# Performance work log

Hardware: AMD Instinct MI355X
Metric: run time of the kernel (lower is better)

Reference implementation:

```python
import jax, jax.numpy as jnp
import numpy as np

NUM_CLASSES = 4
SMOOTH = 1e-05
W_DICE, W_CE, W_BOUND = 1.0, 1.0, 0.01
BIG = 1e8  # effectively-infinite squared distance


def _edt_sq_pass(f, axis):
    # Exact 1D squared-distance transform along `axis` via min-plus:
    # out[i] = min_j f[j] + (i-j)^2  (brute-force O(n^2), fully vectorized)
    n = f.shape[axis]
    i = jnp.arange(n, dtype=f.dtype)
    d2 = (i[:, None] - i[None, :]) ** 2  # [n, n]
    fm = jnp.moveaxis(f, axis, -1)
    out = jnp.min(fm[..., None, :] + d2, axis=-1)
    return jnp.moveaxis(out, -1, axis)


def _edt(zero_mask):
    # Euclidean distance to the nearest True voxel of zero_mask
    # (equivalent to scipy distance_transform_edt(~zero_mask)'s convention:
    #  distance to nearest zero of the input == nearest True of zero_mask).
    f = jnp.where(zero_mask, 0.0, BIG).astype(jnp.float32)
    for ax in range(f.ndim):
        f = _edt_sq_pass(f, ax)
    return jnp.sqrt(f)


def _signed_distance(mask):
    # mask: bool [D,H,W]; signed distance map: + outside, - inside.
    d_out = _edt(mask)            # distance(1 - mask)
    d_in = _edt(~mask)            # distance(mask)
    sdf = d_out - d_in
    total = jnp.sum(mask)
    size = mask.size
    sdf = jnp.where(total == 0, jnp.ones_like(sdf), sdf)
    sdf = jnp.where(total == size, -jnp.ones_like(sdf), sdf)
    return sdf


def setup_inputs() -> dict:
    key = jax.random.key(0)
    k1, k2 = jax.random.split(key)
    preds = jax.random.normal(k1, (4, NUM_CLASSES, 64, 64, 64), dtype=jnp.float32)
    targets = jax.random.randint(k2, (4, 64, 64, 64), 0, NUM_CLASSES, dtype=jnp.int32)
    return {"preds": preds, "targets": targets}


def reference(preds, targets):
    B = preds.shape[0]
    probs = jax.nn.softmax(preds, axis=1)  # [B,C,D,H,W]

    # --- Soft Dice ---
    onehot = jax.nn.one_hot(targets, NUM_CLASSES, dtype=preds.dtype)  # [B,D,H,W,C]
    onehot = jnp.moveaxis(onehot, -1, 1)  # [B,C,D,H,W]
    inter = jnp.sum(probs * onehot, axis=(2, 3, 4))
    union = jnp.sum(probs, axis=(2, 3, 4)) + jnp.sum(onehot, axis=(2, 3, 4))
    dice = (2.0 * inter + SMOOTH) / (union + SMOOTH)
    l_dice = 1.0 - jnp.mean(dice)

    # --- Cross entropy (mean over all voxels) ---
    logp = jax.nn.log_softmax(preds, axis=1)
    picked = jnp.take_along_axis(logp, targets[:, None].astype(jnp.int32), axis=1)
    l_ce = -jnp.mean(picked)

    # --- Boundary loss (classes 1..C-1) ---
    l_bound = jnp.float32(0.0)
    for c in range(1, NUM_CLASSES):
        mask_c = targets == c  # [B,D,H,W]
        sdf_c = jax.vmap(_signed_distance)(mask_c)  # [B,D,H,W]
        l_bound = l_bound + jnp.sum(jnp.mean(sdf_c * probs[:, c], axis=(1, 2, 3)))
    l_bound = l_bound / (B * (NUM_CLASSES - 1))

    return W_DICE * l_dice + W_CE * l_ce + W_BOUND * l_bound
```

## Files before the change

### kernel.cpp

```cpp
#include <hip/hip_runtime.h>
#include <hip/hip_bf16.h>
#include <math.h>

#define NVOX 262144
#define BIGF 1e8f

__device__ __forceinline__ unsigned short f2bf(float x) {
    __hip_bfloat16 h = __float2bfloat16(x);
    return *reinterpret_cast<unsigned short*>(&h);
}
__device__ __forceinline__ float bf2f(unsigned short u) {
    __hip_bfloat16 h = *reinterpret_cast<__hip_bfloat16*>(&u);
    return __bfloat162float(h);
}
__device__ __forceinline__ unsigned short dist2_u16(unsigned long long mask, int w) {
    if (mask == 0ull) return 0xFFFFu;
    unsigned long long mr = mask >> w;
    unsigned long long ml = mask << (63 - w);
    int dr = mr ? __builtin_ctzll(mr) : 127;
    int dl = ml ? __builtin_clzll(ml) : 127;
    int dd = dr < dl ? dr : dl;
    return (unsigned short)(dd * dd);
}

__global__ __launch_bounds__(256) void kA_stats_probs(
    const float* __restrict__ preds, const int* __restrict__ targets,
    unsigned short* __restrict__ probsT, float* __restrict__ part_stats) {
    __shared__ float sred[4 * 13];
    int blk = blockIdx.x;
    int b = blk >> 8, seg = blk & 255;
    int t = threadIdx.x, lane = t & 63, wid = t >> 6;
    size_t vbase = (size_t)seg * 1024 + 4 * t;
    const float* p = preds + (size_t)(b * 4) * NVOX + vbase;
    float4 x0 = *(const float4*)(p);
    float4 x1 = *(const float4*)(p + NVOX);
    float4 x2 = *(const float4*)(p + 2 * NVOX);
    float4 x3 = *(const float4*)(p + 3 * NVOX);
    int4 tv4 = *(const int4*)(targets + (size_t)b * NVOX + vbase);

    float q[13];
    #pragma unroll
    for (int k = 0; k < 13; ++k) q[k] = 0.0f;
    unsigned short pb[3][4];

    #pragma unroll
    for (int j = 0; j < 4; ++j) {
        float a0 = (&x0.x)[j], a1 = (&x1.x)[j], a2 = (&x2.x)[j], a3 = (&x3.x)[j];
        int tv = (&tv4.x)[j];
        float m  = fmaxf(fmaxf(a0, a1), fmaxf(a2, a3));
        float e0 = expf(a0 - m), e1 = expf(a1 - m), e2 = expf(a2 - m), e3 = expf(a3 - m);
        float ssum = e0 + e1 + e2 + e3;
        float inv  = 1.0f / ssum;
        float p0 = e0 * inv, p1 = e1 * inv, p2 = e2 * inv, p3 = e3 * inv;
        float xt = (tv == 0) ? a0 : (tv == 1) ? a1 : (tv == 2) ? a2 : a3;
        q[12] += -(xt - m - logf(ssum));
        q[4] += p0; q[5] += p1; q[6] += p2; q[7] += p3;
        if (tv == 0)      { q[0] += p0; q[8]  += 1.0f; }
        else if (tv == 1) { q[1] += p1; q[9]  += 1.0f; }
        else if (tv == 2) { q[2] += p2; q[10] += 1.0f; }
        else              { q[3] += p3; q[11] += 1.0f; }
        pb[0][j] = f2bf(p1); pb[1][j] = f2bf(p2); pb[2][j] = f2bf(p3);
    }

    int v0 = (int)vbase;
    int d = v0 >> 12, h = (v0 >> 6) & 63, w0 = v0 & 63;
    size_t poff = (size_t)h * 4096 + d * 64 + w0;
    #pragma unroll
    for (int c = 0; c < 3; ++c) {
        ushort4 u = make_ushort4(pb[c][0], pb[c][1], pb[c][2], pb[c][3]);
        *(ushort4*)(probsT + (size_t)(b * 3 + c) * NVOX + poff) = u;
    }

    #pragma unroll
    for (int k = 0; k < 13; ++k) {
        float x = q[k];
        #pragma unroll
        for (int o = 32; o > 0; o >>= 1) x += __shfl_down(x, o);
        if (lane == 0) sred[wid * 13 + k] = x;
    }
    __syncthreads();
    if (t < 13) {
        float s = sred[t] + sred[13 + t] + sred[26 + t] + sred[39 + t];
        part_stats[t * 1024 + blk] = s;
    }
}

__global__ __launch_bounds__(256) void kB_edt12(
    const int* __restrict__ targets, unsigned short* __restrict__ bufA) {
    __shared__ float tO[64 * 65];
    __shared__ float tI[64 * 65];
    int blk = blockIdx.x;
    int cm = blk % 3;
    int bd = blk / 3;
    int d = bd & 63, b = bd >> 6;
    int c = cm + 1;
    int t = threadIdx.x, lane = t & 63, wid = t >> 6;
    const int* tg = targets + (size_t)b * NVOX + (size_t)d * 4096;

    #pragma unroll
    for (int i = 0; i < 16; ++i) {
        int e = t + 256 * i;
        int h = wid + 4 * i;
        int tv = tg[e];
        unsigned long long mask = __ballot(tv == c);
        unsigned short o  = dist2_u16(mask, lane);
        unsigned short ii = dist2_u16(~mask, lane);
        tO[h * 65 + lane] = (o  == 0xFFFFu) ? BIGF : (float)o;
        tI[h * 65 + lane] = (ii == 0xFFFFu) ? BIGF : (float)ii;
    }
    __syncthreads();

    float hf = (float)lane;
    for (int r = 0; r < 16; ++r) {
        int w = wid * 16 + r;
        {
            float best = tO[lane * 65 + w];
            for (int dk = 1; dk < 64; ++dk) {
                float d2 = (float)(dk * dk);
                if (__all(d2 >= best)) break;
                int hl = lane - dk; hl = hl < 0 ? 0 : hl;
                int hr = lane + dk; hr = hr > 63 ? 63 : hr;
                best = fminf(fminf(best, tO[hl * 65 + w] + d2), tO[hr * 65 + w] + d2);
            }
            tO[lane * 65 + w] = best;
        }
        {
            float best = tI[lane * 65 + w];
            for (int dk = 1; dk < 64; ++dk) {
                float d2 = (float)(dk * dk);
                if (__all(d2 >= best)) break;
                int hl = lane - dk; hl = hl < 0 ? 0 : hl;
                int hr = lane + dk; hr = hr > 63 ? 63 : hr;
                best = fminf(fminf(best, tI[hl * 65 + w] + d2), tI[hr * 65 + w] + d2);
            }
            tI[lane * 65 + w] = best;
        }
    }
    __syncthreads();

    int combo = b * 3 + cm;
    size_t oO = (size_t)combo * NVOX + (size_t)d * 64;
    size_t oI = (size_t)(combo + 12) * NVOX + (size_t)d * 64;
    #pragma unroll
    for (int i = 0; i < 16; ++i) {
        int h = wid + 4 * i;
        float vo = tO[h * 65 + lane];
        float vi = tI[h * 65 + lane];
        bufA[oO + (size_t)h * 4096 + lane] = (vo >= 1e7f) ? 0xFFFFu : (unsigned short)vo;
        bufA[oI + (size_t)h * 4096 + lane] = (vi >= 1e7f) ? 0xFFFFu : (unsigned short)vi;
    }
}

__global__ __launch_bounds__(512) void k2_edt3_sdf(
    const unsigned short* __restrict__ bufA, const unsigned short* __restrict__ probsT,
    float* __restrict__ part_bound) {
    __shared__ float pl[2][64 * 65];
    __shared__ float sredb[8];
    int blk = blockIdx.x;
    int combo = blk >> 6, h = blk & 63;
    int t = threadIdx.x, lane = t & 63, wid = t >> 6;

    for (int v = 0; v < 2; ++v) {
        const unsigned short* src = bufA + (size_t)(combo + 12 * v) * NVOX + (size_t)h * 4096;
        #pragma unroll
        for (int i = 0; i < 8; ++i) {
            int e = t + 512 * i;
            unsigned short u = src[e];
            pl[v][e + (e >> 6)] = (u == 0xFFFFu) ? BIGF : (float)u;
        }
    }
    __syncthreads();

    for (int v = 0; v < 2; ++v) {
        for (int r = 0; r < 8; ++r) {
            int w = wid * 8 + r;
            float* col = &pl[v][w];
            float best = col[lane * 65];
            for (int dk = 1; dk < 64; ++dk) {
                float d2 = (float)(dk * dk);
                if (__all(d2 >= best)) break;
                int dl = lane - dk; dl = dl < 0 ? 0 : dl;
                int dr = lane + dk; dr = dr > 63 ? 63 : dr;
                best = fminf(fminf(best, col[dl * 65] + d2), col[dr * 65] + d2);
            }
            col[lane * 65] = best;
        }
    }
    __syncthreads();

    const unsigned short* pp = probsT + (size_t)combo * NVOX + (size_t)h * 4096;
    float acc = 0.0f;
    #pragma unroll
    for (int i = 0; i < 8; ++i) {
        int e = t + 512 * i;
        int li = e + (e >> 6);
        float sdf = sqrtf(pl[0][li]) - sqrtf(pl[1][li]);
        acc += sdf * bf2f(pp[e]);
    }
    #pragma unroll
    for (int o = 32; o > 0; o >>= 1) acc += __shfl_down(acc, o);
    if (lane == 0) sredb[wid] = acc;
    __syncthreads();
    if (t == 0) {
        float s = 0.0f;
        for (int j = 0; j < 8; ++j) s += sredb[j];
        part_bound[blk] = s;
    }
}

__global__ __launch_bounds__(1024) void k3_final(
    const float* __restrict__ part_stats, const float* __restrict__ part_bound,
    float* __restrict__ out) {
    __shared__ float sred[13 * 16];
    __shared__ double S[13 * 4];
    __shared__ double BND[12];
    int t = threadIdx.x, lane = t & 63, wid = t >> 6;

    for (int k = 0; k < 13; ++k) {
        float v = part_stats[k * 1024 + t];
        #pragma unroll
        for (int o = 32; o > 0; o >>= 1) v += __shfl_down(v, o);
        if (lane == 0) sred[k * 16 + wid] = v;
    }
    __syncthreads();
    if (t < 52) {
        int k = t >> 2, b = t & 3;
        double s = (double)sred[k * 16 + b * 4] + (double)sred[k * 16 + b * 4 + 1]
                 + (double)sred[k * 16 + b * 4 + 2] + (double)sred[k * 16 + b * 4 + 3];
        S[k * 4 + b] = s;
    }
    if (t < 768) {
        float v = part_bound[t];
        #pragma unroll
        for (int o = 32; o > 0; o >>= 1) v += __shfl_down(v, o);
        if (lane == 0) BND[wid] = (double)v;
    }
    __syncthreads();
    if (t == 0) {
        const double NV = (double)NVOX;
        double dice_sum = 0.0;
        for (int b = 0; b < 4; ++b)
            for (int c = 0; c < 4; ++c) {
                double inter = S[c * 4 + b];
                double un    = S[(4 + c) * 4 + b] + S[(8 + c) * 4 + b];
                dice_sum += (2.0 * inter + 1e-5) / (un + 1e-5);
            }
        double l_dice = 1.0 - dice_sum / 16.0;
        double l_ce = (S[48] + S[49] + S[50] + S[51]) / (4.0 * NV);
        double lb = 0.0;
        for (int combo = 0; combo < 12; ++combo) {
            int b = combo / 3, c = combo % 3 + 1;
            double cnt = S[(8 + c) * 4 + b];
            double s;
            if (cnt == 0.0)      s =  S[(4 + c) * 4 + b];
            else if (cnt == NV)  s = -S[(4 + c) * 4 + b];
            else                 s =  BND[combo];
            lb += s / NV;
        }
        lb /= 12.0;
        out[0] = (float)(l_dice + l_ce + 0.01 * lb);
    }
}

extern "C" void kernel_launch(void* const* d_in, const int* in_sizes, int n_in,
                              void* d_out, int out_size, void* d_ws, size_t ws_size,
                              hipStream_t stream) {
    const float* preds   = (const float*)d_in[0];
    const int*   targets = (const int*)d_in[1];
    float* out = (float*)d_out;

    unsigned short* bufA   = (unsigned short*)d_ws;
    unsigned short* probsT = bufA + (size_t)24 * NVOX;
    float* part_stats = (float*)(probsT + (size_t)12 * NVOX);
    float* part_bound = part_stats + 13 * 1024;

    kA_stats_probs<<<1024, 256, 0, stream>>>(preds, targets, probsT, part_stats);
    kB_edt12<<<768, 256, 0, stream>>>(targets, bufA);
    k2_edt3_sdf<<<768, 512, 0, stream>>>(bufA, probsT, part_bound);
    k3_final<<<1, 1024, 0, stream>>>(part_stats, part_bound, out);
}
```

Before: 55.81 us.

## Merge independent stage kernels and fold final reduction into last-block epilogue

Result: slower. 164.1 us (+194.1%).

```diff
diff --git a/kernel.cpp b/kernel.cpp
--- a/kernel.cpp
+++ b/kernel.cpp
@@ -4,6 +4,9 @@
 
 #define NVOX 262144
 #define BIGF 1e8f
+#define GRID_A 1024
+#define GRID_B 768
+#define GRID_K2 768
 
 __device__ __forceinline__ unsigned short f2bf(float x) {
     __hip_bfloat16 h = __float2bfloat16(x);
@@ -23,139 +26,141 @@
     return (unsigned short)(dd * dd);
 }
 
-__global__ __launch_bounds__(256) void kA_stats_probs(
+__global__ __launch_bounds__(256) void K1_fused(
     const float* __restrict__ preds, const int* __restrict__ targets,
-    unsigned short* __restrict__ probsT, float* __restrict__ part_stats) {
-    __shared__ float sred[4 * 13];
-    int blk = blockIdx.x;
-    int b = blk >> 8, seg = blk & 255;
-    int t = threadIdx.x, lane = t & 63, wid = t >> 6;
-    size_t vbase = (size_t)seg * 1024 + 4 * t;
-    const float* p = preds + (size_t)(b * 4) * NVOX + vbase;
-    float4 x0 = *(const float4*)(p);
-    float4 x1 = *(const float4*)(p + NVOX);
-    float4 x2 = *(const float4*)(p + 2 * NVOX);
-    float4 x3 = *(const float4*)(p + 3 * NVOX);
-    int4 tv4 = *(const int4*)(targets + (size_t)b * NVOX + vbase);
-
-    float q[13];
-    #pragma unroll
-    for (int k = 0; k < 13; ++k) q[k] = 0.0f;
-    unsigned short pb[3][4];
-
-    #pragma unroll
-    for (int j = 0; j < 4; ++j) {
-        float a0 = (&x0.x)[j], a1 = (&x1.x)[j], a2 = (&x2.x)[j], a3 = (&x3.x)[j];
-        int tv = (&tv4.x)[j];
-        float m  = fmaxf(fmaxf(a0, a1), fmaxf(a2, a3));
-        float e0 = expf(a0 - m), e1 = expf(a1 - m), e2 = expf(a2 - m), e3 = expf(a3 - m);
-        float ssum = e0 + e1 + e2 + e3;
-        float inv  = 1.0f / ssum;
-        float p0 = e0 * inv, p1 = e1 * inv, p2 = e2 * inv, p3 = e3 * inv;
-        float xt = (tv == 0) ? a0 : (tv == 1) ? a1 : (tv == 2) ? a2 : a3;
-        q[12] += -(xt - m - logf(ssum));
-        q[4] += p0; q[5] += p1; q[6] += p2; q[7] += p3;
-        if (tv == 0)      { q[0] += p0; q[8]  += 1.0f; }
-        else if (tv == 1) { q[1] += p1; q[9]  += 1.0f; }
-        else if (tv == 2) { q[2] += p2; q[10] += 1.0f; }
-        else              { q[3] += p3; q[11] += 1.0f; }
-        pb[0][j] = f2bf(p1); pb[1][j] = f2bf(p2); pb[2][j] = f2bf(p3);
-    }
-
-    int v0 = (int)vbase;
-    int d = v0 >> 12, h = (v0 >> 6) & 63, w0 = v0 & 63;
-    size_t poff = (size_t)h * 4096 + d * 64 + w0;
-    #pragma unroll
-    for (int c = 0; c < 3; ++c) {
-        ushort4 u = make_ushort4(pb[c][0], pb[c][1], pb[c][2], pb[c][3]);
-        *(ushort4*)(probsT + (size_t)(b * 3 + c) * NVOX + poff) = u;
-    }
-
-    #pragma unroll
-    for (int k = 0; k < 13; ++k) {
-        float x = q[k];
-        #pragma unroll
-        for (int o = 32; o > 0; o >>= 1) x += __shfl_down(x, o);
-        if (lane == 0) sred[wid * 13 + k] = x;
-    }
-    __syncthreads();
-    if (t < 13) {
-        float s = sred[t] + sred[13 + t] + sred[26 + t] + sred[39 + t];
-        part_stats[t * 1024 + blk] = s;
-    }
-}
-
-__global__ __launch_bounds__(256) void kB_edt12(
-    const int* __restrict__ targets, unsigned short* __restrict__ bufA) {
+    unsigned short* __restrict__ bufA, unsigned short* __restrict__ probsT,
+    float* __restrict__ part_stats, int* __restrict__ counter) {
     __shared__ float tO[64 * 65];
     __shared__ float tI[64 * 65];
-    int blk = blockIdx.x;
-    int cm = blk % 3;
-    int bd = blk / 3;
-    int d = bd & 63, b = bd >> 6;
-    int c = cm + 1;
+    __shared__ float sred[4 * 13];
+    int bid = blockIdx.x;
     int t = threadIdx.x, lane = t & 63, wid = t >> 6;
-    const int* tg = targets + (size_t)b * NVOX + (size_t)d * 4096;
-
-    #pragma unroll
-    for (int i = 0; i < 16; ++i) {
-        int e = t + 256 * i;
-        int h = wid + 4 * i;
-        int tv = tg[e];
-        unsigned long long mask = __ballot(tv == c);
-        unsigned short o  = dist2_u16(mask, lane);
-        unsigned short ii = dist2_u16(~mask, lane);
-        tO[h * 65 + lane] = (o  == 0xFFFFu) ? BIGF : (float)o;
-        tI[h * 65 + lane] = (ii == 0xFFFFu) ? BIGF : (float)ii;
-    }
-    __syncthreads();
-
-    float hf = (float)lane;
-    for (int r = 0; r < 16; ++r) {
-        int w = wid * 16 + r;
-        {
-            float best = tO[lane * 65 + w];
-            for (int dk = 1; dk < 64; ++dk) {
-                float d2 = (float)(dk * dk);
-                if (__all(d2 >= best)) break;
-                int hl = lane - dk; hl = hl < 0 ? 0 : hl;
-                int hr = lane + dk; hr = hr > 63 ? 63 : hr;
-                best = fminf(fminf(best, tO[hl * 65 + w] + d2), tO[hr * 65 + w] + d2);
-            }
-            tO[lane * 65 + w] = best;
-        }
-        {
-            float best = tI[lane * 65 + w];
-            for (int dk = 1; dk < 64; ++dk) {
-                float d2 = (float)(dk * dk);
-                if (__all(d2 >= best)) break;
-                int hl = lane - dk; hl = hl < 0 ? 0 : hl;
-                int hr = lane + dk; hr = hr > 63 ? 63 : hr;
-                best = fminf(fminf(best, tI[hl * 65 + w] + d2), tI[hr * 65 + w] + d2);
-            }
-            tI[lane * 65 + w] = best;
-        }
-    }
-    __syncthreads();
-
-    int combo = b * 3 + cm;
-    size_t oO = (size_t)combo * NVOX + (size_t)d * 64;
-    size_t oI = (size_t)(combo + 12) * NVOX + (size_t)d * 64;
-    #pragma unroll
-    for (int i = 0; i < 16; ++i) {
-        int h = wid + 4 * i;
-        float vo = tO[h * 65 + lane];
-        float vi = tI[h * 65 + lane];
-        bufA[oO + (size_t)h * 4096 + lane] = (vo >= 1e7f) ? 0xFFFFu : (unsigned short)vo;
-        bufA[oI + (size_t)h * 4096 + lane] = (vi >= 1e7f) ? 0xFFFFu : (unsigned short)vi;
-    }
-}
-
-__global__ __launch_bounds__(512) void k2_edt3_sdf(
+
+    if (bid < GRID_A) {
+        if (bid == 0 && t == 0) *counter = 0;
+        int b = bid >> 8, seg = bid & 255;
+        size_t vbase = (size_t)seg * 1024 + 4 * t;
+        const float* p = preds + (size_t)(b * 4) * NVOX + vbase;
+        float4 x0 = *(const float4*)(p);
+        float4 x1 = *(const float4*)(p + NVOX);
+        float4 x2 = *(const float4*)(p + 2 * NVOX);
+        float4 x3 = *(const float4*)(p + 3 * NVOX);
+        int4 tv4 = *(const int4*)(targets + (size_t)b * NVOX + vbase);
+
+        float q[13];
+        #pragma unroll
+        for (int k = 0; k < 13; ++k) q[k] = 0.0f;
+        unsigned short pb[3][4];
+
+        #pragma unroll
+        for (int j = 0; j < 4; ++j) {
+            float a0 = (&x0.x)[j], a1 = (&x1.x)[j], a2 = (&x2.x)[j], a3 = (&x3.x)[j];
+            int tv = (&tv4.x)[j];
+            float m  = fmaxf(fmaxf(a0, a1), fmaxf(a2, a3));
+            float e0 = expf(a0 - m), e1 = expf(a1 - m), e2 = expf(a2 - m), e3 = expf(a3 - m);
+            float ssum = e0 + e1 + e2 + e3;
+            float inv  = 1.0f / ssum;
+            float p0 = e0 * inv, p1 = e1 * inv, p2 = e2 * inv, p3 = e3 * inv;
+            float xt = (tv == 0) ? a0 : (tv == 1) ? a1 : (tv == 2) ? a2 : a3;
+            q[12] += -(xt - m - logf(ssum));
+            q[4] += p0; q[5] += p1; q[6] += p2; q[7] += p3;
+            if (tv == 0)      { q[0] += p0; q[8]  += 1.0f; }
+            else if (tv == 1) { q[1] += p1; q[9]  += 1.0f; }
+            else if (tv == 2) { q[2] += p2; q[10] += 1.0f; }
+            else              { q[3] += p3; q[11] += 1.0f; }
+            pb[0][j] = f2bf(p1); pb[1][j] = f2bf(p2); pb[2][j] = f2bf(p3);
+        }
+
+        int v0 = (int)vbase;
+        int d = v0 >> 12, h = (v0 >> 6) & 63, w0 = v0 & 63;
+        size_t poff = (size_t)h * 4096 + d * 64 + w0;
+        #pragma unroll
+        for (int c = 0; c < 3; ++c) {
+            ushort4 u = make_ushort4(pb[c][0], pb[c][1], pb[c][2], pb[c][3]);
+            *(ushort4*)(probsT + (size_t)(b * 3 + c) * NVOX + poff) = u;
+        }
+
+        #pragma unroll
+        for (int k = 0; k < 13; ++k) {
+            float x = q[k];
+            #pragma unroll
+            for (int o = 32; o > 0; o >>= 1) x += __shfl_down(x, o);
+            if (lane == 0) sred[wid * 13 + k] = x;
+        }
+        __syncthreads();
+        if (t < 13) {
+            float s = sred[t] + sred[13 + t] + sred[26 + t] + sred[39 + t];
+            part_stats[t * 1024 + bid] = s;
+        }
+    } else {
+        int blk = bid - GRID_A;
+        int cm = blk % 3;
+        int bd = blk / 3;
+        int d = bd & 63, b = bd >> 6;
+        int c = cm + 1;
+        const int* tg = targets + (size_t)b * NVOX + (size_t)d * 4096;
+
+        #pragma unroll
+        for (int i = 0; i < 16; ++i) {
+            int e = t + 256 * i;
+            int h = wid + 4 * i;
+            int tv = tg[e];
+            unsigned long long mask = __ballot(tv == c);
+            unsigned short o  = dist2_u16(mask, lane);
+            unsigned short ii = dist2_u16(~mask, lane);
+            tO[h * 65 + lane] = (o  == 0xFFFFu) ? BIGF : (float)o;
+            tI[h * 65 + lane] = (ii == 0xFFFFu) ? BIGF : (float)ii;
+        }
+        __syncthreads();
+
+        for (int r = 0; r < 16; ++r) {
+            int w = wid * 16 + r;
+            {
+                float best = tO[lane * 65 + w];
+                for (int dk = 1; dk < 64; ++dk) {
+                    float d2 = (float)(dk * dk);
+                    if (__all(d2 >= best)) break;
+                    int hl = lane - dk; hl = hl < 0 ? 0 : hl;
+                    int hr = lane + dk; hr = hr > 63 ? 63 : hr;
+                    best = fminf(fminf(best, tO[hl * 65 + w] + d2), tO[hr * 65 + w] + d2);
+                }
+                tO[lane * 65 + w] = best;
+            }
+            {
+                float best = tI[lane * 65 + w];
+                for (int dk = 1; dk < 64; ++dk) {
+                    float d2 = (float)(dk * dk);
+                    if (__all(d2 >= best)) break;
+                    int hl = lane - dk; hl = hl < 0 ? 0 : hl;
+                    int hr = lane + dk; hr = hr > 63 ? 63 : hr;
+                    best = fminf(fminf(best, tI[hl * 65 + w] + d2), tI[hr * 65 + w] + d2);
+                }
+                tI[lane * 65 + w] = best;
+            }
+        }
+        __syncthreads();
+
+        int combo = b * 3 + cm;
+        size_t oO = (size_t)combo * NVOX + (size_t)d * 64;
+        size_t oI = (size_t)(combo + 12) * NVOX + (size_t)d * 64;
+        #pragma unroll
+        for (int i = 0; i < 16; ++i) {
+            int h = wid + 4 * i;
+            float vo = tO[h * 65 + lane];
+            float vi = tI[h * 65 + lane];
+            bufA[oO + (size_t)h * 4096 + lane] = (vo >= 1e7f) ? 0xFFFFu : (unsigned short)vo;
+            bufA[oI + (size_t)h * 4096 + lane] = (vi >= 1e7f) ? 0xFFFFu : (unsigned short)vi;
+        }
+    }
+}
+
+__global__ __launch_bounds__(512) void K2_fused(
     const unsigned short* __restrict__ bufA, const unsigned short* __restrict__ probsT,
-    float* __restrict__ part_bound) {
+    const float* __restrict__ part_stats, float* __restrict__ part_bound,
+    int* __restrict__ counter, float* __restrict__ out) {
     __shared__ float pl[2][64 * 65];
     __shared__ float sredb[8];
+    __shared__ int amLast;
     int blk = blockIdx.x;
     int combo = blk >> 6, h = blk & 63;
     int t = threadIdx.x, lane = t & 63, wid = t >> 6;
@@ -206,34 +211,35 @@
         for (int j = 0; j < 8; ++j) s += sredb[j];
         part_bound[blk] = s;
     }
-}
-
-__global__ __launch_bounds__(1024) void k3_final(
-    const float* __restrict__ part_stats, const float* __restrict__ part_bound,
-    float* __restrict__ out) {
-    __shared__ float sred[13 * 16];
-    __shared__ double S[13 * 4];
+
+    __threadfence();
+    if (t == 0) amLast = (atomicAdd(counter, 1) == GRID_K2 - 1);
+    __syncthreads();
+    if (!amLast) return;
+    __threadfence();
+
+    __shared__ float csred[13 * 8];
+    __shared__ double S[52];
     __shared__ double BND[12];
-    int t = threadIdx.x, lane = t & 63, wid = t >> 6;
-
     for (int k = 0; k < 13; ++k) {
-        float v = part_stats[k * 1024 + t];
+        int b = t >> 7, s = t & 127;
+        float v = part_stats[k * 1024 + b * 256 + s]
+                + part_stats[k * 1024 + b * 256 + s + 128];
         #pragma unroll
         for (int o = 32; o > 0; o >>= 1) v += __shfl_down(v, o);
-        if (lane == 0) sred[k * 16 + wid] = v;
+        if (lane == 0) csred[k * 8 + wid] = v;
     }
     __syncthreads();
     if (t < 52) {
         int k = t >> 2, b = t & 3;
-        double s = (double)sred[k * 16 + b * 4] + (double)sred[k * 16 + b * 4 + 1]
-                 + (double)sred[k * 16 + b * 4 + 2] + (double)sred[k * 16 + b * 4 + 3];
-        S[k * 4 + b] = s;
-    }
-    if (t < 768) {
-        float v = part_bound[t];
-        #pragma unroll
-        for (int o = 32; o > 0; o >>= 1) v += __shfl_down(v, o);
-        if (lane == 0) BND[wid] = (double)v;
+        S[k * 4 + b] = (double)csred[k * 8 + b * 2] + (double)csred[k * 8 + b * 2 + 1];
+    }
+    if (wid < 6) {
+        float v1 = part_bound[wid * 64 + lane];
+        float v2 = part_bound[(wid + 6) * 64 + lane];
+        #pragma unroll
+        for (int o = 32; o > 0; o >>= 1) { v1 += __shfl_down(v1, o); v2 += __shfl_down(v2, o); }
+        if (lane == 0) { BND[wid] = (double)v1; BND[wid + 6] = (double)v2; }
     }
     __syncthreads();
     if (t == 0) {
@@ -248,13 +254,13 @@
         double l_dice = 1.0 - dice_sum / 16.0;
         double l_ce = (S[48] + S[49] + S[50] + S[51]) / (4.0 * NV);
         double lb = 0.0;
-        for (int combo = 0; combo < 12; ++combo) {
-            int b = combo / 3, c = combo % 3 + 1;
+        for (int cb = 0; cb < 12; ++cb) {
+            int b = cb / 3, c = cb % 3 + 1;
             double cnt = S[(8 + c) * 4 + b];
             double s;
             if (cnt == 0.0)      s =  S[(4 + c) * 4 + b];
             else if (cnt == NV)  s = -S[(4 + c) * 4 + b];
-            else                 s =  BND[combo];
+            else                 s =  BND[cb];
             lb += s / NV;
         }
         lb /= 12.0;
@@ -273,9 +279,10 @@
     unsigned short* probsT = bufA + (size_t)24 * NVOX;
     float* part_stats = (float*)(probsT + (size_t)12 * NVOX);
     float* part_bound = part_stats + 13 * 1024;
-
-    kA_stats_probs<<<1024, 256, 0, stream>>>(preds, targets, probsT, part_stats);
-    kB_edt12<<<768, 256, 0, stream>>>(targets, bufA);
-    k2_edt3_sdf<<<768, 512, 0, stream>>>(bufA, probsT, part_bound);
-    k3_final<<<1, 1024, 0, stream>>>(part_stats, part_bound, out);
-}
+    int*   counter    = (int*)(part_bound + GRID_K2);
+
+    K1_fused<<<GRID_A + GRID_B, 256, 0, stream>>>(preds, targets, bufA, probsT,
+                                                  part_stats, counter);
+    K2_fused<<<GRID_K2, 512, 0, stream>>>(bufA, probsT, part_stats, part_bound,
+                                          counter, out);
+}
```
